# Performance work log

Measured on AMD Instinct MI355X. Metric: run time of the kernel, lower is better.

## Reference

```python
import jax, jax.numpy as jnp
import numpy as np

B, T, V, D, U, NT = 32, 512, 32000, 300, 300, 3


def setup_inputs() -> dict:
    key = jax.random.key(0)
    ks = jax.random.split(key, 10)
    s = 0.05
    return {
        "inputs": jax.random.randint(ks[0], (B, T), 0, V),
        "sequence_length": jax.random.randint(ks[1], (B,), 0, T),
        "emb": jax.random.normal(ks[2], (V, D), jnp.float32) * s,
        "Wk_f": jax.random.normal(ks[3], (D, 4 * U), jnp.float32) * s,
        "Wr_f": jax.random.normal(ks[4], (U, 4 * U), jnp.float32) * s,
        "b_f": jnp.zeros((4 * U,), jnp.float32),
        "Wk_b": jax.random.normal(ks[5], (D, 4 * U), jnp.float32) * s,
        "Wr_b": jax.random.normal(ks[6], (U, 4 * U), jnp.float32) * s,
        "b_b": jnp.zeros((4 * U,), jnp.float32),
        "fc_W": jax.random.normal(ks[7], (2 * U, NT), jnp.float32) * s,
        "fc_b": jnp.zeros((NT,), jnp.float32),
    }


def _lstm_scan(x, mask, Wk, Wr, b):
    # x: [B,T,D], mask: [B,T] bool. Keras semantics: masked steps carry h,c through.
    units = Wr.shape[0]
    zx = jnp.einsum('btd,dz->btz', x, Wk) + b        # precompute input projection
    zx_t = jnp.swapaxes(zx, 0, 1)                    # [T,B,4U]
    m_t = jnp.swapaxes(mask, 0, 1)                   # [T,B]

    def step(carry, inp):
        h, c = carry
        zxt, mt = inp
        z = zxt + h @ Wr                             # [B,4U]
        i, f, g, o = jnp.split(z, 4, axis=-1)
        c_new = jax.nn.sigmoid(f) * c + jax.nn.sigmoid(i) * jnp.tanh(g)
        h_new = jax.nn.sigmoid(o) * jnp.tanh(c_new)
        m = mt[:, None]
        h = jnp.where(m, h_new, h)
        c = jnp.where(m, c_new, c)
        return (h, c), h

    h0 = jnp.zeros((x.shape[0], units), x.dtype)
    _, hs = jax.lax.scan(step, (h0, h0), (zx_t, m_t))
    return jnp.swapaxes(hs, 0, 1)                    # [B,T,U]


def reference(inputs, sequence_length, emb, Wk_f, Wr_f, b_f, Wk_b, Wr_b, b_b, fc_W, fc_b):
    x = emb[inputs]                                   # [B,T,D]
    mask = jnp.arange(T)[None, :] < sequence_length[:, None]  # [B,T]
    h_fwd = _lstm_scan(x, mask, Wk_f, Wr_f, b_f)
    # backward direction: reverse time (input + mask), scan, reverse output back
    h_bwd = jnp.flip(_lstm_scan(jnp.flip(x, 1), jnp.flip(mask, 1), Wk_b, Wr_b, b_b), 1)
    h = jnp.concatenate([h_fwd, h_bwd], axis=-1)      # [B,T,2U]
    return h @ fc_W + fc_b                            # [B,T,NT]
```

## Files before the change

kernel.cpp:

```cpp
#include <hip/hip_runtime.h>
#include <stdint.h>


#define BB 32
#define TT 512
#define DD 300
#define UU 300
#define G4 1200
#define NTOK 3

#define KB   10
#define UPB  30
#define NCOL 120
#define KTILES 10
#define HSTR 320
#define HROW 304

#define WKROWS 1280
#define WKSTR  320

typedef uint16_t bf16_t;
typedef short  s16x8 __attribute__((ext_vector_type(8)));
typedef float  f32x4 __attribute__((ext_vector_type(4)));

union U8 { unsigned long long q[2]; s16x8 v; };

__device__ __forceinline__ float bf2f(uint16_t u) {
    union { uint32_t i; float f; } v; v.i = ((uint32_t)u) << 16; return v.f;
}
__device__ __forceinline__ uint16_t f2bf(float f) {
    union { uint32_t i; float f; } v; v.f = f;
    uint32_t r = v.i + 0x7fffu + ((v.i >> 16) & 1u);
    return (uint16_t)(r >> 16);
}
__device__ __forceinline__ float ldf(const void* base, size_t idx, int f32m) {
    return f32m ? ((const float*)base)[idx]
                : bf2f(((const uint16_t*)base)[idx]);
}

__device__ __forceinline__ f32x4 xpose4(f32x4 v, int lane) {
    f32x4 t, w, s, r;
    t[0] = __shfl_xor(v[0], 1); t[1] = __shfl_xor(v[1], 1);
    t[2] = __shfl_xor(v[2], 1); t[3] = __shfl_xor(v[3], 1);
    if ((lane & 1) == 0) { w[0]=v[0]; w[1]=t[0]; w[2]=v[2]; w[3]=t[2]; }
    else                 { w[0]=t[1]; w[1]=v[1]; w[2]=t[3]; w[3]=v[3]; }
    s[0] = __shfl_xor(w[0], 2); s[1] = __shfl_xor(w[1], 2);
    s[2] = __shfl_xor(w[2], 2); s[3] = __shfl_xor(w[3], 2);
    if ((lane & 2) == 0) { r[0]=w[0]; r[1]=w[1]; r[2]=s[0]; r[3]=s[1]; }
    else                 { r[0]=s[2]; r[1]=s[3]; r[2]=w[2]; r[3]=w[3]; }
    return r;
}

__device__ __forceinline__ float fsig(float x) {
    return __builtin_amdgcn_rcpf(1.f + __expf(-x));
}
__device__ __forceinline__ float ftanh(float x) {
    float cx = fminf(10.f, fmaxf(-10.f, x));
    float e = __expf(2.f * cx);
    return (e - 1.f) * __builtin_amdgcn_rcpf(e + 1.f);
}

__device__ __forceinline__ void gatefn(f32x4 zv, uint2 zp, bool m,
                                       float& c, float& h) {
    float zi = zv[0] + bf2f((uint16_t)(zp.x & 0xffff));
    float zf = zv[1] + bf2f((uint16_t)(zp.x >> 16));
    float zg = zv[2] + bf2f((uint16_t)(zp.y & 0xffff));
    float zo = zv[3] + bf2f((uint16_t)(zp.y >> 16));
    float si = fsig(zi);
    float sf = fsig(zf);
    float so = fsig(zo);
    float tg = ftanh(zg);
    float cn = sf * c + si * tg;
    float hn = so * ftanh(cn);
    if (m) { c = cn; h = hn; }
}

__global__ void detect_dtype(const uint16_t* __restrict__ emb_u16,
                             int* __restrict__ flag) {
    __shared__ float red[256];
    const int tid = threadIdx.x;
    float m = 0.f;
    for (int k = tid; k < 4096; k += 256)
        m = fmaxf(m, fabsf(bf2f(emb_u16[2 * k])));
    red[tid] = m;
    __syncthreads();
    for (int s = 128; s > 0; s >>= 1) {
        if (tid < s) red[tid] = fmaxf(red[tid], red[tid + s]);
        __syncthreads();
    }
    if (tid == 0) flag[0] = (red[0] > 1.0e3f) ? 1 : 0;
}

__global__ void prep_wrp(const void* __restrict__ Wr_f,
                         const void* __restrict__ Wr_b,
                         bf16_t* __restrict__ WrPT_f,
                         bf16_t* __restrict__ WrPT_b,
                         const int* __restrict__ flagp) {
    const int f32m = *flagp;
    int idx = blockIdx.x * 256 + threadIdx.x;
    const void* src = blockIdx.y ? Wr_b : Wr_f;
    bf16_t*     dst = blockIdx.y ? WrPT_b : WrPT_f;
    if (idx < G4 * HROW) {
        int p = idx / HROW;
        int k = idx - p * HROW;
        int u = p >> 2, g = p & 3;
        float v = (k < DD) ? ldf(src, (size_t)k * G4 + g * UU + u, f32m) : 0.f;
        dst[idx] = f2bf(v);
    }
}

__global__ void prep_wkt(const void* __restrict__ Wk_f, const void* __restrict__ b_f,
                         const void* __restrict__ Wk_b, const void* __restrict__ b_b,
                         bf16_t* __restrict__ WkT, bf16_t* __restrict__ biasP,
                         const int* __restrict__ flagp) {
    const int f32m = *flagp;
    const int dir = blockIdx.y;
    const void* Wk = dir ? Wk_b : Wk_f;
    const void* bs = dir ? b_b  : b_f;
    bf16_t* dst = WkT + (size_t)dir * (WKROWS * WKSTR);
    int idx = blockIdx.x * 256 + threadIdx.x;
    if (idx < WKROWS * WKSTR) {
        int p = idx / WKSTR;
        int k = idx - p * WKSTR;
        int u = p >> 2, g = p & 3;
        float v = (p < G4 && k < DD) ? ldf(Wk, (size_t)k * G4 + g * UU + u, f32m)
                                     : 0.f;
        dst[idx] = f2bf(v);
        if (idx < WKROWS) {
            int pp = idx, uu = pp >> 2, gg = pp & 3;
            biasP[dir * WKROWS + idx] =
                (pp < G4) ? f2bf(ldf(bs, gg * UU + uu, f32m)) : (bf16_t)0;
        }
    }
}

__global__ void init_state(bf16_t* __restrict__ Hglob, int* __restrict__ flags) {
    int i = blockIdx.x * 256 + threadIdx.x;
    if (i < 2 * 2 * BB * HROW) Hglob[i] = 0;
    if (i < 2 * TT * 16) flags[i] = 0;
}

#define ZM 64
#define ZN 128
__global__ __launch_bounds__(256, 2) void zx_gemm3(
    const int* __restrict__ inputs, const void* __restrict__ emb,
    const bf16_t* __restrict__ WkTall, const bf16_t* __restrict__ biasP,
    bf16_t* __restrict__ zxf, bf16_t* __restrict__ zxb,
    const int* __restrict__ flagp) {

    const int f32m = *flagp;
    const int dir = blockIdx.y;
    const bf16_t* WkT = WkTall + (size_t)dir * (WKROWS * WKSTR);
    const bf16_t* bp  = biasP + dir * WKROWS;
    bf16_t* out = dir ? zxb : zxf;

    const int tid = threadIdx.x;
    const int rowBase = blockIdx.x * ZM;

    __shared__ __align__(16) uint16_t Alds[ZM * HSTR];
    __shared__ int rowids[ZM];

    if (tid < ZM) rowids[tid] = inputs[rowBase + tid];
    for (int i = tid; i < ZM * HSTR; i += 256) Alds[i] = 0;
    __syncthreads();

    for (int i = tid; i < ZM * 38; i += 256) {
        int r = i / 38, g = i - 38 * r;
        int k0 = g * 8;
        const size_t eb = (size_t)rowids[r] * DD + k0;
        uint16_t tmp[8];
        if (g < 37) {
            if (f32m) {
                const float* ef = (const float*)emb + eb;
#pragma unroll
                for (int e = 0; e < 8; e++) tmp[e] = f2bf(ef[e]);
            } else {
                *(uint4*)tmp = *(const uint4*)((const uint16_t*)emb + eb);
            }
        } else {
#pragma unroll
            for (int e = 0; e < 8; e++) {
                int k = k0 + e;
                tmp[e] = (k < DD)
                    ? (f32m ? f2bf(((const float*)emb)[(size_t)rowids[r] * DD + k])
                            : ((const uint16_t*)emb)[(size_t)rowids[r] * DD + k])
                    : (uint16_t)0;
            }
        }
        *(uint4*)&Alds[r * HSTR + ((g ^ (r & 7)) << 3)] = *(uint4*)tmp;
    }
    __syncthreads();

    const int lane = tid & 63;
    const int wv   = tid >> 6;
    const int q    = lane >> 4;
    const int c16  = lane & 15;
    const int n0   = 32 * wv;
    const int sw7  = c16 & 7;
    const bool evn = ((lane & 1) == 0);

    for (int nt = 0; nt < 10; nt++) {
        const int pb = nt * ZN;
        const int p0 = pb + n0 + c16;
        const int p1 = p0 + 16;
        const float bv0 = bf2f(bp[p0]);
        const float bv1 = bf2f(bp[p1]);

        f32x4 acc[4][2];
#pragma unroll
        for (int mt = 0; mt < 4; mt++)
            for (int nh = 0; nh < 2; nh++) acc[mt][nh] = (f32x4){0.f,0.f,0.f,0.f};

#pragma unroll
        for (int kt = 0; kt < KTILES; kt++) {
            int k0 = 32 * kt + 8 * q;
            int sw = (((kt * 4 + q) ^ sw7) << 3);
            s16x8 b0 = *(const s16x8*)&WkT[(size_t)p0 * WKSTR + k0];
            s16x8 b1 = *(const s16x8*)&WkT[(size_t)p1 * WKSTR + k0];
#pragma unroll
            for (int mt = 0; mt < 4; mt++) {
                s16x8 af = *(const s16x8*)&Alds[(16 * mt + c16) * HSTR + sw];
                acc[mt][0] = __builtin_amdgcn_mfma_f32_16x16x32_bf16(af, b0, acc[mt][0], 0, 0, 0);
                acc[mt][1] = __builtin_amdgcn_mfma_f32_16x16x32_bf16(af, b1, acc[mt][1], 0, 0, 0);
            }
        }

#pragma unroll
        for (int mt = 0; mt < 4; mt++) {
#pragma unroll
            for (int nh = 0; nh < 2; nh++) {
                const int p = (nh == 0) ? p0 : p1;
                const float bv = (nh == 0) ? bv0 : bv1;
#pragma unroll
                for (int r = 0; r < 4; r++) {
                    uint32_t mine = f2bf(acc[mt][nh][r] + bv);
                    uint32_t other = (uint32_t)__shfl_xor((int)mine, 1);
                    if (evn && p < G4) {
                        uint32_t pk = mine | (other << 16);
                        int row = rowBase + 16 * mt + 4 * q + r;
                        *(uint32_t*)&out[(size_t)row * G4 + p] = pk;
                    }
                }
            }
        }
    }
}

__global__ __launch_bounds__(256, 1) void lstm_rec4(
    const bf16_t* __restrict__ zxf, const bf16_t* __restrict__ zxb,
    const bf16_t* __restrict__ WrPT_f, const bf16_t* __restrict__ WrPT_b,
    const int* __restrict__ seqlen,
    bf16_t* __restrict__ Hglob, int* __restrict__ flags,
    bf16_t* __restrict__ hf, bf16_t* __restrict__ hb) {

    const int blk = blockIdx.x % KB;
    const int dir = blockIdx.x / KB;
    const bf16_t* zx   = dir ? zxb    : zxf;
    const bf16_t* WrPT = dir ? WrPT_b : WrPT_f;
    bf16_t*       hout = dir ? hb : hf;
    bf16_t*       Hg   = Hglob + (size_t)dir * (2 * BB * HROW);
    int*          fbase = flags + dir * (TT * 16);

    __shared__ __align__(16) uint16_t Hlds[BB * HSTR];
    __shared__ uint16_t hstage[BB * UPB];

    const int tid  = threadIdx.x;
    const int lane = tid & 63;
    const int wv   = tid >> 6;
    const int q    = lane >> 4;
    const int c16  = lane & 15;
    const int n0   = 32 * wv;
    const int sw7  = c16 & 7;
    const int k4   = c16 >> 2;
    const int j4   = c16 & 3;
    const int u0   = 8 * wv + k4;
    const int b0   = 4 * q + j4;
    const bool v1  = (u0 + 4 < UPB);
    const bool pollme = (lane < KB) && (lane != blk);

    for (int i = tid; i < BB * HSTR; i += 256) Hlds[i] = 0;
    U8 Bf0[KTILES], Bf1[KTILES];
#pragma unroll
    for (int kt = 0; kt < KTILES; kt++) {
        int k0 = 32 * kt + 8 * q;
        int col0 = n0 + c16, col1 = n0 + 16 + c16;
        U8 z; z.q[0] = 0; z.q[1] = 0;
        Bf0[kt] = z; Bf1[kt] = z;
        if (k0 < 304) {
            if (col0 < NCOL)
                Bf0[kt].v = *(const s16x8*)&WrPT[(size_t)(NCOL * blk + col0) * HROW + k0];
            if (col1 < NCOL)
                Bf1[kt].v = *(const s16x8*)&WrPT[(size_t)(NCOL * blk + col1) * HROW + k0];
        }
    }
    float c00 = 0.f, c01 = 0.f, c10 = 0.f, c11 = 0.f;
    float h00 = 0.f, h01 = 0.f, h10 = 0.f, h11 = 0.f;
    const int L0 = seqlen[b0];
    const int L1 = seqlen[b0 + 16];
    __syncthreads();

    for (int ts = 0; ts < TT; ts++) {
        const int t = dir ? (TT - 1 - ts) : ts;

        const size_t zr0 = ((size_t)(b0 * TT + t)) * G4 + NCOL * blk;
        const size_t zr1 = ((size_t)((b0 + 16) * TT + t)) * G4 + NCOL * blk;
        uint2 z00 = *(const uint2*)&zx[zr0 + 4 * u0];
        uint2 z10 = *(const uint2*)&zx[zr1 + 4 * u0];
        uint2 z01 = {0, 0}, z11 = {0, 0};
        if (v1) {
            z01 = *(const uint2*)&zx[zr0 + 4 * (u0 + 4)];
            z11 = *(const uint2*)&zx[zr1 + 4 * (u0 + 4)];
        }

        if (ts > 0) {
            int* fl = fbase + (ts - 1) * 16;
            int a = pollme ? __hip_atomic_load(&fl[lane], __ATOMIC_RELAXED,
                                               __HIP_MEMORY_SCOPE_AGENT) : 1;
            if (!__all(a != 0)) {
                int b = pollme ? __hip_atomic_load(&fl[lane], __ATOMIC_RELAXED,
                                                   __HIP_MEMORY_SCOPE_AGENT) : 1;
                int c = pollme ? __hip_atomic_load(&fl[lane], __ATOMIC_RELAXED,
                                                   __HIP_MEMORY_SCOPE_AGENT) : 1;
                for (;;) {
                    if (__all(a != 0)) break;
                    a = b; b = c;
                    c = pollme ? __hip_atomic_load(&fl[lane], __ATOMIC_RELAXED,
                                                   __HIP_MEMORY_SCOPE_AGENT) : 1;
                }
            }
        }

        const unsigned long long* Hsrc64 =
            (const unsigned long long*)(Hg + (size_t)(ts & 1) * (BB * HROW));
        unsigned long long hv[10];
#pragma unroll
        for (int k = 0; k < 9; k++)
            hv[k] = __hip_atomic_load(&Hsrc64[tid + 256 * k], __ATOMIC_RELAXED,
                                      __HIP_MEMORY_SCOPE_AGENT);
        if (tid < 128)
            hv[9] = __hip_atomic_load(&Hsrc64[2304 + tid], __ATOMIC_RELAXED,
                                      __HIP_MEMORY_SCOPE_AGENT);
#pragma unroll
        for (int k = 0; k < 9; k++) {
            int i = tid + 256 * k;
            int b = i / 76, x = i - 76 * b;
            *(unsigned long long*)
                &Hlds[b * HSTR + ((((x >> 1) ^ (b & 7)) << 3) | ((x & 1) << 2))]
                = hv[k];
        }
        if (tid < 128) {
            int i = 2304 + tid;
            int b = i / 76, x = i - 76 * b;
            *(unsigned long long*)
                &Hlds[b * HSTR + ((((x >> 1) ^ (b & 7)) << 3) | ((x & 1) << 2))]
                = hv[9];
        }
        __syncthreads();

        f32x4 acc00 = {0.f,0.f,0.f,0.f}, acc01 = {0.f,0.f,0.f,0.f};
        f32x4 acc10 = {0.f,0.f,0.f,0.f}, acc11 = {0.f,0.f,0.f,0.f};
#pragma unroll
        for (int kt = 0; kt < KTILES; kt++) {
            int sw = (((kt * 4 + q) ^ sw7) << 3);
            s16x8 a0 = *(const s16x8*)&Hlds[c16 * HSTR + sw];
            s16x8 a1 = *(const s16x8*)&Hlds[(c16 + 16) * HSTR + sw];
            acc00 = __builtin_amdgcn_mfma_f32_16x16x32_bf16(a0, Bf0[kt].v, acc00, 0, 0, 0);
            acc01 = __builtin_amdgcn_mfma_f32_16x16x32_bf16(a0, Bf1[kt].v, acc01, 0, 0, 0);
            acc10 = __builtin_amdgcn_mfma_f32_16x16x32_bf16(a1, Bf0[kt].v, acc10, 0, 0, 0);
            acc11 = __builtin_amdgcn_mfma_f32_16x16x32_bf16(a1, Bf1[kt].v, acc11, 0, 0, 0);
        }

        f32x4 t00 = xpose4(acc00, lane);
        f32x4 t01 = xpose4(acc01, lane);
        f32x4 t10 = xpose4(acc10, lane);
        f32x4 t11 = xpose4(acc11, lane);
        const bool m0 = (t < L0);
        const bool m1 = (t < L1);
        gatefn(t00, z00, m0, c00, h00);
        gatefn(t01, z01, m0, c01, h01);
        gatefn(t10, z10, m1, c10, h10);
        gatefn(t11, z11, m1, c11, h11);

        hstage[b0 * UPB + u0]        = f2bf(h00);
        hstage[(b0 + 16) * UPB + u0] = f2bf(h10);
        if (v1) {
            hstage[b0 * UPB + u0 + 4]        = f2bf(h01);
            hstage[(b0 + 16) * UPB + u0 + 4] = f2bf(h11);
        }
        __syncthreads();

        if (ts < TT - 1) {
            bf16_t* Hdst = Hg + (size_t)((ts + 1) & 1) * (BB * HROW);
            for (int i = tid; i < BB * (UPB / 2); i += 256) {
                int b = i / (UPB / 2), k = i - b * (UPB / 2);
                uint32_t val = (uint32_t)hstage[b * UPB + 2 * k] |
                               ((uint32_t)hstage[b * UPB + 2 * k + 1] << 16);
                __hip_atomic_store(
                    (uint32_t*)&Hdst[b * HROW + UPB * blk + 2 * k], val,
                    __ATOMIC_RELAXED, __HIP_MEMORY_SCOPE_AGENT);
            }
            __syncthreads();
            if (tid == 0)
                __hip_atomic_store(&fbase[ts * 16 + blk], 1, __ATOMIC_RELAXED,
                                   __HIP_MEMORY_SCOPE_AGENT);
        }

        for (int i = tid; i < BB * (UPB / 2); i += 256) {
            int b = i / (UPB / 2), k = i - b * (UPB / 2);
            uint32_t val = (uint32_t)hstage[b * UPB + 2 * k] |
                           ((uint32_t)hstage[b * UPB + 2 * k + 1] << 16);
            *(uint32_t*)&hout[((size_t)(b * TT + t)) * UU + UPB * blk + 2 * k] = val;
        }
    }
}

__global__ __launch_bounds__(256) void fc_out(
    const bf16_t* __restrict__ hf, const bf16_t* __restrict__ hb,
    const void* __restrict__ fcW, const void* __restrict__ fcb,
    void* __restrict__ out, const int* __restrict__ flagp) {

    const int f32m = *flagp;
    __shared__ float W[2 * UU * NTOK];
    __shared__ float bias[NTOK];
    const int tid = threadIdx.x;
    for (int i = tid; i < 2 * UU * NTOK; i += 256) W[i] = ldf(fcW, i, f32m);
    if (tid < NTOK) bias[tid] = ldf(fcb, tid, f32m);
    __syncthreads();

    const int r = blockIdx.x * 256 + tid;
    const bf16_t* hfr = hf + (size_t)r * UU;
    const bf16_t* hbr = hb + (size_t)r * UU;
    float s0 = bias[0], s1 = bias[1], s2 = bias[2];
    for (int u = 0; u < UU; u++) {
        float f = bf2f(hfr[u]);
        s0 += f * W[u * 3 + 0];
        s1 += f * W[u * 3 + 1];
        s2 += f * W[u * 3 + 2];
    }
    for (int u = 0; u < UU; u++) {
        float f = bf2f(hbr[u]);
        s0 += f * W[(UU + u) * 3 + 0];
        s1 += f * W[(UU + u) * 3 + 1];
        s2 += f * W[(UU + u) * 3 + 2];
    }
    if (f32m) {
        float* o = (float*)out;
        o[(size_t)r * 3 + 0] = s0;
        o[(size_t)r * 3 + 1] = s1;
        o[(size_t)r * 3 + 2] = s2;
    } else {
        bf16_t* o = (bf16_t*)out;
        o[(size_t)r * 3 + 0] = f2bf(s0);
        o[(size_t)r * 3 + 1] = f2bf(s1);
        o[(size_t)r * 3 + 2] = f2bf(s2);
    }
}

extern "C" void kernel_launch(void* const* d_in, const int* in_sizes, int n_in,
                              void* d_out, int out_size, void* d_ws, size_t ws_size,
                              hipStream_t stream) {
    const int* inputs = (const int*)d_in[0];
    const int* seqlen = (const int*)d_in[1];
    const void* emb  = d_in[2];
    const void* Wk_f = d_in[3];
    const void* Wr_f = d_in[4];
    const void* b_f  = d_in[5];
    const void* Wk_b = d_in[6];
    const void* Wr_b = d_in[7];
    const void* b_b  = d_in[8];
    const void* fcW  = d_in[9];
    const void* fcb  = d_in[10];

    char* ws = (char*)d_ws;
    int*    flag   = (int*)(ws + 0);
    int*    flags  = (int*)(ws + 64);
    bf16_t* Hglob  = (bf16_t*)(ws + 65664);
    bf16_t* WrPT_f = (bf16_t*)(ws + 143488);
    bf16_t* WrPT_b = (bf16_t*)(ws + 873088);
    bf16_t* zxPf   = (bf16_t*)(ws + 1602688);
    bf16_t* zxPb   = (bf16_t*)(ws + 40924288);
    bf16_t* hfbuf  = (bf16_t*)(ws + 80245888);
    bf16_t* hbbuf  = (bf16_t*)(ws + 90076288);
    bf16_t* WkT    = hfbuf;
    bf16_t* biasP  = hfbuf + 2 * WKROWS * WKSTR;

    detect_dtype<<<1, 256, 0, stream>>>((const uint16_t*)emb, flag);
    {
        dim3 grid((G4 * HROW + 255) / 256, 2);
        prep_wrp<<<grid, 256, 0, stream>>>(Wr_f, Wr_b, WrPT_f, WrPT_b, flag);
    }
    {
        dim3 grid((WKROWS * WKSTR + 255) / 256, 2);
        prep_wkt<<<grid, 256, 0, stream>>>(Wk_f, b_f, Wk_b, b_b, WkT, biasP, flag);
    }
    init_state<<<64, 256, 0, stream>>>(Hglob, flags);
    {
        dim3 grid(256, 2);
        zx_gemm3<<<grid, 256, 0, stream>>>(inputs, emb, WkT, biasP,
                                           zxPf, zxPb, flag);
    }
    lstm_rec4<<<2 * KB, 256, 0, stream>>>(zxPf, zxPb, WrPT_f, WrPT_b, seqlen,
                                          Hglob, flags, hfbuf, hbbuf);
    fc_out<<<(BB * TT) / 256, 256, 0, stream>>>(hfbuf, hbbuf, fcW, fcb,
                                                d_out, flag);
}
```

Baseline: 1.723 ms.

## Replace per-step flag barrier with tagged hidden-state words in LSTM recurrence

Each exchanged 64-bit word now carries a bf16 pair of hidden values in its low half and the timestep in its high half. Consumers spin until every word they read has the expected tag, so the separate flag array, the extra block barrier and the flag store per step are gone. Producers write straight from registers after a lane shuffle instead of going through the LDS staging buffer. The cost is twice the bytes per exchanged value and a reread of the whole hidden-state tile on each failed poll.

```diff
diff --git a/kernel.cpp b/kernel.cpp
--- a/kernel.cpp
+++ b/kernel.cpp
@@ -18,6 +18,10 @@
 
 #define WKROWS 1280
 #define WKSTR  320
+
+#define WPR  150
+#define WBUF (BB * WPR)
+#define PW   19
 
 typedef uint16_t bf16_t;
 typedef short  s16x8 __attribute__((ext_vector_type(8)));
@@ -134,10 +138,9 @@
     }
 }
 
-__global__ void init_state(bf16_t* __restrict__ Hglob, int* __restrict__ flags) {
+__global__ void init_state(unsigned long long* __restrict__ Hw) {
     int i = blockIdx.x * 256 + threadIdx.x;
-    if (i < 2 * 2 * BB * HROW) Hglob[i] = 0;
-    if (i < 2 * TT * 16) flags[i] = 0;
+    if (i < 2 * 2 * WBUF) Hw[i] = 0ull;
 }
 
 #define ZM 64
@@ -246,11 +249,11 @@
     }
 }
 
-__global__ __launch_bounds__(256, 1) void lstm_rec4(
+__global__ __launch_bounds__(256, 1) void lstm_rec8(
     const bf16_t* __restrict__ zxf, const bf16_t* __restrict__ zxb,
     const bf16_t* __restrict__ WrPT_f, const bf16_t* __restrict__ WrPT_b,
     const int* __restrict__ seqlen,
-    bf16_t* __restrict__ Hglob, int* __restrict__ flags,
+    unsigned long long* __restrict__ Hw,
     bf16_t* __restrict__ hf, bf16_t* __restrict__ hb) {
 
     const int blk = blockIdx.x % KB;
@@ -258,8 +261,7 @@
     const bf16_t* zx   = dir ? zxb    : zxf;
     const bf16_t* WrPT = dir ? WrPT_b : WrPT_f;
     bf16_t*       hout = dir ? hb : hf;
-    bf16_t*       Hg   = Hglob + (size_t)dir * (2 * BB * HROW);
-    int*          fbase = flags + dir * (TT * 16);
+    unsigned long long* const Hwd = Hw + (size_t)dir * (2 * WBUF);
 
     __shared__ __align__(16) uint16_t Hlds[BB * HSTR];
     __shared__ uint16_t hstage[BB * UPB];
@@ -276,7 +278,17 @@
     const int u0   = 8 * wv + k4;
     const int b0   = 4 * q + j4;
     const bool v1  = (u0 + 4 < UPB);
-    const bool pollme = (lane < KB) && (lane != blk);
+
+    int Wl[PW], El[PW];
+#pragma unroll
+    for (int m = 0; m < PW; ++m) {
+        int W = tid + 256 * m;
+        if (W >= WBUF) W = tid;
+        int b = W / WPR, w = W - WPR * b;
+        int u = 2 * w, g = u >> 3;
+        Wl[m] = W;
+        El[m] = b * HSTR + ((g ^ (b & 7)) << 3) + (u & 7);
+    }
 
     for (int i = tid; i < BB * HSTR; i += 256) Hlds[i] = 0;
     U8 Bf0[KTILES], Bf1[KTILES];
@@ -313,47 +325,25 @@
         }
 
         if (ts > 0) {
-            int* fl = fbase + (ts - 1) * 16;
-            int a = pollme ? __hip_atomic_load(&fl[lane], __ATOMIC_RELAXED,
-                                               __HIP_MEMORY_SCOPE_AGENT) : 1;
-            if (!__all(a != 0)) {
-                int b = pollme ? __hip_atomic_load(&fl[lane], __ATOMIC_RELAXED,
-                                                   __HIP_MEMORY_SCOPE_AGENT) : 1;
-                int c = pollme ? __hip_atomic_load(&fl[lane], __ATOMIC_RELAXED,
-                                                   __HIP_MEMORY_SCOPE_AGENT) : 1;
-                for (;;) {
-                    if (__all(a != 0)) break;
-                    a = b; b = c;
-                    c = pollme ? __hip_atomic_load(&fl[lane], __ATOMIC_RELAXED,
-                                                   __HIP_MEMORY_SCOPE_AGENT) : 1;
+            const unsigned long long* const src = Hwd + (size_t)(ts & 1) * WBUF;
+            const uint32_t tagv = (uint32_t)ts;
+            unsigned long long hv[PW];
+            for (;;) {
+#pragma unroll
+                for (int m = 0; m < PW; ++m)
+                    hv[m] = __hip_atomic_load(&src[Wl[m]], __ATOMIC_RELAXED,
+                                              __HIP_MEMORY_SCOPE_AGENT);
+                bool ok = true;
+#pragma unroll
+                for (int m = 0; m < PW; ++m)
+                    ok &= ((uint32_t)(hv[m] >> 32) == tagv);
+                if (__all(ok)) {
+#pragma unroll
+                    for (int m = 0; m < PW; ++m)
+                        *(uint32_t*)&Hlds[El[m]] = (uint32_t)hv[m];
+                    break;
                 }
             }
-        }
-
-        const unsigned long long* Hsrc64 =
-            (const unsigned long long*)(Hg + (size_t)(ts & 1) * (BB * HROW));
-        unsigned long long hv[10];
-#pragma unroll
-        for (int k = 0; k < 9; k++)
-            hv[k] = __hip_atomic_load(&Hsrc64[tid + 256 * k], __ATOMIC_RELAXED,
-                                      __HIP_MEMORY_SCOPE_AGENT);
-        if (tid < 128)
-            hv[9] = __hip_atomic_load(&Hsrc64[2304 + tid], __ATOMIC_RELAXED,
-                                      __HIP_MEMORY_SCOPE_AGENT);
-#pragma unroll
-        for (int k = 0; k < 9; k++) {
-            int i = tid + 256 * k;
-            int b = i / 76, x = i - 76 * b;
-            *(unsigned long long*)
-                &Hlds[b * HSTR + ((((x >> 1) ^ (b & 7)) << 3) | ((x & 1) << 2))]
-                = hv[k];
-        }
-        if (tid < 128) {
-            int i = 2304 + tid;
-            int b = i / 76, x = i - 76 * b;
-            *(unsigned long long*)
-                &Hlds[b * HSTR + ((((x >> 1) ^ (b & 7)) << 3) | ((x & 1) << 2))]
-                = hv[9];
         }
         __syncthreads();
 
@@ -381,6 +371,33 @@
         gatefn(t10, z10, m1, c10, h10);
         gatefn(t11, z11, m1, c11, h11);
 
+        if (ts < TT - 1) {
+            unsigned long long* const dst = Hwd + (size_t)((ts + 1) & 1) * WBUF;
+            const unsigned long long tg =
+                ((unsigned long long)(uint32_t)(ts + 1)) << 32;
+            float p00 = __shfl_xor(h00, 4);
+            float p10 = __shfl_xor(h10, 4);
+            float p01 = __shfl_xor(h01, 4);
+            float p11 = __shfl_xor(h11, 4);
+            if ((k4 & 1) == 0) {
+                const int gw0 = 15 * blk + 4 * wv + (k4 >> 1);
+                uint32_t q00 = (uint32_t)f2bf(h00) | ((uint32_t)f2bf(p00) << 16);
+                uint32_t q10 = (uint32_t)f2bf(h10) | ((uint32_t)f2bf(p10) << 16);
+                __hip_atomic_store(&dst[b0 * WPR + gw0], tg | q00,
+                                   __ATOMIC_RELAXED, __HIP_MEMORY_SCOPE_AGENT);
+                __hip_atomic_store(&dst[(b0 + 16) * WPR + gw0], tg | q10,
+                                   __ATOMIC_RELAXED, __HIP_MEMORY_SCOPE_AGENT);
+                if (v1) {
+                    uint32_t q01 = (uint32_t)f2bf(h01) | ((uint32_t)f2bf(p01) << 16);
+                    uint32_t q11 = (uint32_t)f2bf(h11) | ((uint32_t)f2bf(p11) << 16);
+                    __hip_atomic_store(&dst[b0 * WPR + gw0 + 2], tg | q01,
+                                       __ATOMIC_RELAXED, __HIP_MEMORY_SCOPE_AGENT);
+                    __hip_atomic_store(&dst[(b0 + 16) * WPR + gw0 + 2], tg | q11,
+                                       __ATOMIC_RELAXED, __HIP_MEMORY_SCOPE_AGENT);
+                }
+            }
+        }
+
         hstage[b0 * UPB + u0]        = f2bf(h00);
         hstage[(b0 + 16) * UPB + u0] = f2bf(h10);
         if (v1) {
@@ -388,22 +405,6 @@
             hstage[(b0 + 16) * UPB + u0 + 4] = f2bf(h11);
         }
         __syncthreads();
-
-        if (ts < TT - 1) {
-            bf16_t* Hdst = Hg + (size_t)((ts + 1) & 1) * (BB * HROW);
-            for (int i = tid; i < BB * (UPB / 2); i += 256) {
-                int b = i / (UPB / 2), k = i - b * (UPB / 2);
-                uint32_t val = (uint32_t)hstage[b * UPB + 2 * k] |
-                               ((uint32_t)hstage[b * UPB + 2 * k + 1] << 16);
-                __hip_atomic_store(
-                    (uint32_t*)&Hdst[b * HROW + UPB * blk + 2 * k], val,
-                    __ATOMIC_RELAXED, __HIP_MEMORY_SCOPE_AGENT);
-            }
-            __syncthreads();
-            if (tid == 0)
-                __hip_atomic_store(&fbase[ts * 16 + blk], 1, __ATOMIC_RELAXED,
-                                   __HIP_MEMORY_SCOPE_AGENT);
-        }
 
         for (int i = tid; i < BB * (UPB / 2); i += 256) {
             int b = i / (UPB / 2), k = i - b * (UPB / 2);
@@ -473,14 +474,13 @@
 
     char* ws = (char*)d_ws;
     int*    flag   = (int*)(ws + 0);
-    int*    flags  = (int*)(ws + 64);
-    bf16_t* Hglob  = (bf16_t*)(ws + 65664);
-    bf16_t* WrPT_f = (bf16_t*)(ws + 143488);
-    bf16_t* WrPT_b = (bf16_t*)(ws + 873088);
-    bf16_t* zxPf   = (bf16_t*)(ws + 1602688);
-    bf16_t* zxPb   = (bf16_t*)(ws + 40924288);
-    bf16_t* hfbuf  = (bf16_t*)(ws + 80245888);
-    bf16_t* hbbuf  = (bf16_t*)(ws + 90076288);
+    unsigned long long* Hw = (unsigned long long*)(ws + 64);
+    bf16_t* WrPT_f = (bf16_t*)(ws + 153664);
+    bf16_t* WrPT_b = (bf16_t*)(ws + 883264);
+    bf16_t* zxPf   = (bf16_t*)(ws + 1612864);
+    bf16_t* zxPb   = (bf16_t*)(ws + 40934464);
+    bf16_t* hfbuf  = (bf16_t*)(ws + 80256064);
+    bf16_t* hbbuf  = (bf16_t*)(ws + 90086464);
     bf16_t* WkT    = hfbuf;
     bf16_t* biasP  = hfbuf + 2 * WKROWS * WKSTR;
 
@@ -493,14 +493,14 @@
         dim3 grid((WKROWS * WKSTR + 255) / 256, 2);
         prep_wkt<<<grid, 256, 0, stream>>>(Wk_f, b_f, Wk_b, b_b, WkT, biasP, flag);
     }
-    init_state<<<64, 256, 0, stream>>>(Hglob, flags);
+    init_state<<<75, 256, 0, stream>>>(Hw);
     {
         dim3 grid(256, 2);
         zx_gemm3<<<grid, 256, 0, stream>>>(inputs, emb, WkT, biasP,
                                            zxPf, zxPb, flag);
     }
-    lstm_rec4<<<2 * KB, 256, 0, stream>>>(zxPf, zxPb, WrPT_f, WrPT_b, seqlen,
-                                          Hglob, flags, hfbuf, hbbuf);
+    lstm_rec8<<<2 * KB, 256, 0, stream>>>(zxPf, zxPb, WrPT_f, WrPT_b, seqlen,
+                                          Hw, hfbuf, hbbuf);
     fc_out<<<(BB * TT) / 256, 256, 0, stream>>>(hfbuf, hbbuf, fcW, fcb,
                                                 d_out, flag);
 }
```

Measured after the change: 1.908 ms. 10.7% more time.
